# Performance work log

Measured on AMD Instinct MI355X. Metric: run time of the kernel, lower is better.

The kernel has to match this reference:

```python
import jax, jax.numpy as jnp
import numpy as np

B, T, N, DIN, U, K, C = 32, 256, 128, 16, 64, 2, 4
M = K + 1  # num diffusion matrices per support (I, P, 2P^2-I, ...)


def setup_inputs() -> dict:
    key = jax.random.key(0)
    ks = jax.random.split(key, 10)
    w = lambda k, shape: jax.random.normal(k, shape, jnp.float32) * 0.05
    inp = {}
    inp["input_seq"] = jax.random.normal(ks[0], (B, T, N, DIN), jnp.float32)
    inp["seq_lengths"] = jax.random.randint(ks[1], (B,), 1, T + 1)
    # scaled dense support (graph laplacian surrogate) for numerical stability
    inp["support"] = jax.random.normal(ks[2], (N, N), jnp.float32) / N
    inp["W0_gate"] = w(ks[3], ((DIN + U) * M, 2 * U))
    inp["b0_gate"] = jnp.ones((2 * U,), jnp.float32)  # bias_start=1.0
    inp["W0_cand"] = w(ks[4], ((DIN + U) * M, U))
    inp["b0_cand"] = jnp.zeros((U,), jnp.float32)
    inp["W1_gate"] = w(ks[5], (2 * U * M, 2 * U))
    inp["b1_gate"] = jnp.ones((2 * U,), jnp.float32)
    inp["W1_cand"] = w(ks[6], (2 * U * M, U))
    inp["b1_cand"] = jnp.zeros((U,), jnp.float32)
    inp["W_fc"] = w(ks[7], (U, C))
    inp["b_fc"] = jnp.zeros((C,), jnp.float32)
    return inp


def _gconv(x, support, W, b):
    # x: (B, N, Cin). Chebyshev-style diffusion: [x, Px, 2P(Px)-x, ...]
    x0 = x
    x1 = jnp.einsum('mn,bnc->bmc', support, x0)
    xs = [x0, x1]
    for _ in range(2, K + 1):
        x2 = 2.0 * jnp.einsum('mn,bnc->bmc', support, x1) - x0
        xs.append(x2)
        x0, x1 = x1, x2
    # stack on last axis -> (B, N, Cin, M) -> (B, N, Cin*M), matching the
    # torch reshape order (input feature major, matrix minor)
    xc = jnp.stack(xs, axis=-1).reshape(x.shape[0], x.shape[1], -1)
    return xc @ W + b


def _cell(x, h, support, Wg, bg, Wc, bc):
    # x: (B,N,Din), h: (B,N,U)
    val = jax.nn.sigmoid(_gconv(jnp.concatenate([x, h], axis=-1), support, Wg, bg))
    r, u = jnp.split(val, 2, axis=-1)
    c = jnp.tanh(_gconv(jnp.concatenate([x, r * h], axis=-1), support, Wc, bc))
    return u * h + (1.0 - u) * c


def _run_layer(x_seq, support, Wg, bg, Wc, bc):
    # x_seq: (T, B, N, D)
    def step(h, x):
        h2 = _cell(x, h, support, Wg, bg, Wc, bc)
        return h2, h2
    h0 = jnp.zeros((x_seq.shape[1], N, U), x_seq.dtype)
    _, out = jax.lax.scan(step, h0, x_seq)
    return out  # (T, B, N, U)


def reference(input_seq, seq_lengths, support, W0_gate, b0_gate, W0_cand, b0_cand,
              W1_gate, b1_gate, W1_cand, b1_cand, W_fc, b_fc):
    x = jnp.transpose(input_seq, (1, 0, 2, 3))  # (T,B,N,DIN)
    h1 = _run_layer(x, support, W0_gate, b0_gate, W0_cand, b0_cand)
    h2 = _run_layer(h1, support, W1_gate, b1_gate, W1_cand, b1_cand)
    out_seq = jnp.transpose(h2, (1, 0, 2, 3))  # (B,T,N,U)
    idx = seq_lengths - 1  # last relevant timestep per sequence
    last = out_seq[jnp.arange(out_seq.shape[0]), idx]  # (B,N,U)
    # dropout is identity in eval mode
    logits = jax.nn.relu(last) @ W_fc + b_fc  # (B,N,C)
    return jnp.max(logits, axis=1)  # max-pool over nodes -> (B,C)
```

## Files before the change

### kernel.cpp

```cpp
#include <hip/hip_runtime.h>

#define B_   32
#define T_   256
#define N_   128
#define DIN_ 16
#define U_   64

#define PD 456
#define PT 136
#define LDS_BYTES ((N_*PD + N_*PT)*2)

#define WT0G_OFF 0
#define WT0C_OFF (128*256)
#define WT1G_OFF (WT0C_OFF + 64*256)
#define WT1C_OFF (WT1G_OFF + 128*384)
#define WT_TOTAL (WT1C_OFF + 64*384)
#define S2_OFF   WT_TOTAL
#define FIFO_OFF (S2_OFF + 128*128)
#define FIFO_SLOT(bb,tt) (FIFO_OFF + ((bb)*8 + ((tt)&7))*8192)
#define FLG_BYTE ((FIFO_OFF + 32*8*8192)*2)

typedef __attribute__((ext_vector_type(8))) short bfrag;
typedef __attribute__((ext_vector_type(4))) float ffrag;
typedef __attribute__((ext_vector_type(4))) unsigned short us4;
typedef __attribute__((ext_vector_type(2))) unsigned short us2;
typedef unsigned long long ull;

#define SYNC() asm volatile("s_waitcnt lgkmcnt(0)\n\ts_barrier" ::: "memory")
#define MFMA16(a,b,c) __builtin_amdgcn_mfma_f32_16x16x32_bf16(a,b,c,0,0,0)

__device__ __forceinline__ unsigned short f2b(float x) {
  union { float f; unsigned u; } v; v.f = x;
  return (unsigned short)((v.u + 0x7fffu + ((v.u >> 16) & 1u)) >> 16);
}
__device__ __forceinline__ float sigm(float x) {
  float e = __expf(-x);
  return __builtin_amdgcn_rcpf(1.f + e);
}
__device__ __forceinline__ float tanh_(float x) {
  float e = __expf(2.f * x);
  return 1.f - 2.f * __builtin_amdgcn_rcpf(1.f + e);
}

__device__ __forceinline__ float wval0(const float* w, int ncol, int co, int k) {
  if (k < 16)  return w[(k*3+0)*ncol+co] - w[(k*3+2)*ncol+co];
  if (k < 48)  { int j=k-16, c=j>>1;
                 return (j&1) ? 2.f*w[(c*3+2)*ncol+co] : w[(c*3+1)*ncol+co]; }
  if (k < 64)  return 0.f;
  if (k < 128) { int c=16+(k-64); return w[(c*3+0)*ncol+co] - w[(c*3+2)*ncol+co]; }
  { int j=k-128, c=16+(j>>1);
    return (j&1) ? 2.f*w[(c*3+2)*ncol+co] : w[(c*3+1)*ncol+co]; }
}
__device__ __forceinline__ float wval1(const float* w, int ncol, int co, int k) {
  if (k < 64)  return w[(k*3+0)*ncol+co] - w[(k*3+2)*ncol+co];
  if (k < 192) { int j=k-64, c=j>>1;
                 return (j&1) ? 2.f*w[(c*3+2)*ncol+co] : w[(c*3+1)*ncol+co]; }
  if (k < 256) { int c=64+(k-192); return w[(c*3+0)*ncol+co] - w[(c*3+2)*ncol+co]; }
  { int j=k-256, c=64+(j>>1);
    return (j&1) ? 2.f*w[(c*3+2)*ncol+co] : w[(c*3+1)*ncol+co]; }
}
__device__ __forceinline__ float wval0c(const float* w, int ncol, int co, int k) {
  if (k < 64)  return wval0(w, ncol, co, k);
  if (k < 192) return wval0(w, ncol, co, k + 64);
  return wval0(w, ncol, co, k - 128);
}
__device__ __forceinline__ float wval1c(const float* w, int ncol, int co, int k) {
  if (k < 192) return wval1(w, ncol, co, k);
  if (k < 320) return wval1(w, ncol, co, k + 64);
  return wval1(w, ncol, co, k - 128);
}

__global__ void setup_wt(const float* __restrict__ w0g, const float* __restrict__ w0c,
                         const float* __restrict__ w1g, const float* __restrict__ w1c,
                         unsigned short* __restrict__ wt) {
  int i = blockIdx.x * blockDim.x + threadIdx.x;
  if (i >= WT_TOTAL) return;
  float v;
  if (i < WT0C_OFF)      { int co = i >> 8, k = i & 255;                 v = wval0 (w0g, 128, co, k); }
  else if (i < WT1G_OFF) { int j = i - WT0C_OFF; v = wval0c(w0c, 64, j >> 8, j & 255); }
  else if (i < WT1C_OFF) { int j = i - WT1G_OFF; v = wval1 (w1g, 128, j / 384, j % 384); }
  else                   { int j = i - WT1C_OFF; v = wval1c(w1c, 64, j / 384, j % 384); }
  wt[i] = f2b(v);
}

__global__ void setup_s2(const float* __restrict__ sup, unsigned short* __restrict__ s2) {
  int idx = blockIdx.x * blockDim.x + threadIdx.x;
  int i = idx >> 7, j = idx & 127;
  float acc = 0.f;
#pragma unroll 4
  for (int k = 0; k < 128; ++k) acc += sup[i*128 + k] * sup[k*128 + j];
  s2[idx] = f2b(acc);
}

__global__ void zero_flags(unsigned short* __restrict__ wt) {
  int* flg = (int*)((char*)wt + FLG_BYTE);
  if (threadIdx.x < 64) flg[threadIdx.x] = 0;
}

template<int KT>
__device__ __forceinline__ void gateR(ffrag (&acc)[4][2],
    const bfrag (&bwr)[KT], const bfrag (&bwu)[KT],
    const unsigned short* __restrict__ arowB, const int lq) {
#pragma unroll
  for (int ks = 0; ks < KT; ++ks) {
    bfrag a[4];
#pragma unroll
    for (int i = 0; i < 4; ++i)
      a[i] = *(const bfrag*)&arowB[16*i*PD + 32*ks + 8*lq];
#pragma unroll
    for (int i = 0; i < 4; ++i) {
      acc[i][0] = MFMA16(a[i], bwr[ks], acc[i][0]);
      acc[i][1] = MFMA16(a[i], bwu[ks], acc[i][1]);
    }
  }
}
template<int KT>
__device__ __forceinline__ void candR(ffrag (&acc)[4], bfrag (&bw)[4],
    const unsigned short* __restrict__ arowB, const int (&kofs)[KT],
    const unsigned short* __restrict__ bpc, const int lq) {
#pragma unroll
  for (int ks = 0; ks < KT; ++ks) {
    const int k = ks & 3;
    bfrag a[4];
#pragma unroll
    for (int i = 0; i < 4; ++i)
      a[i] = *(const bfrag*)&arowB[16*i*PD + kofs[ks] + 8*lq];
    bfrag bc = bw[k];
    if (ks + 4 < KT) bw[k] = *(const bfrag*)&bpc[32*(ks+4) + 8*lq];
#pragma unroll
    for (int i = 0; i < 4; ++i) acc[i] = MFMA16(a[i], bc, acc[i]);
  }
}

__global__ __launch_bounds__(512, 2) void dcgru(
    const float* __restrict__ xseq, const int* __restrict__ slen,
    const float* __restrict__ sup,
    const float* __restrict__ b0g, const float* __restrict__ b0c,
    const float* __restrict__ b1g, const float* __restrict__ b1c,
    const float* __restrict__ wfc, const float* __restrict__ bfc,
    unsigned short* __restrict__ wt, float* __restrict__ out) {
  extern __shared__ unsigned short lds[];
  unsigned short* diffb = lds;
  unsigned short* difT  = lds + N_*PD;
  const int b    = (blockIdx.x & 7) | ((blockIdx.x >> 4) << 3);
  const int eta  = (blockIdx.x >> 3) & 1;
  const int tid  = threadIdx.x;
  const int w    = tid >> 6;
  const int j    = w & 3;
  const int g    = w >> 2;
  const int ln   = tid & 15;
  const int lq   = (tid >> 4) & 3;
  const int L    = slen[b];
  int* flg  = (int*)((char*)wt + FLG_BYTE);
  int* prod = flg + b;
  int* cons = flg + 32 + b;
  const unsigned short* __restrict__ arowB = diffb + (64*g + ln)*PD;
  const ffrag fz = {0.f, 0.f, 0.f, 0.f};

  bfrag Sf[4], S2f[4];
#pragma unroll
  for (int ks = 0; ks < 4; ++ks) {
    const float* pS = sup + (16*w + ln)*N_ + 32*ks + 8*lq;
    union { bfrag v; unsigned short u[8]; } tmp;
#pragma unroll
    for (int jj = 0; jj < 8; ++jj) tmp.u[jj] = f2b(pS[jj]);
    Sf[ks] = tmp.v;
    S2f[ks] = *(const bfrag*)&wt[S2_OFF + (16*w + ln)*N_ + 32*ks + 8*lq];
  }

  auto diffuse = [&](int nt, int colc) {
    bfrag bf[4];
#pragma unroll
    for (int ks = 0; ks < 4; ++ks)
      bf[ks] = *(const bfrag*)&difT[(16*nt + ln)*PT + 32*ks + 8*lq];
    ffrag a1 = fz, a2 = fz;
#pragma unroll
    for (int ks = 0; ks < 4; ++ks) {
      a1 = MFMA16(Sf[ks],  bf[ks], a1);
      a2 = MFMA16(S2f[ks], bf[ks], a2);
    }
    const int n0 = 16*w + 4*lq;
    const int col = colc + 2*ln;
#pragma unroll
    for (int r = 0; r < 4; ++r) {
      us2 pq = {f2b(a1[r]), f2b(a2[r])};
      *(us2*)&diffb[(n0 + r)*PD + col] = pq;
    }
  };
  auto dumpCell = [&](ffrag (&v)[4], int colBase, int rowBase) {
    const int chh = 16*j + ln;
#pragma unroll
    for (int i = 0; i < 4; ++i) {
      const int n0 = 64*g + 16*i + 4*lq;
      unsigned short sv[4];
#pragma unroll
      for (int r = 0; r < 4; ++r) sv[r] = f2b(v[i][r]);
#pragma unroll
      for (int r = 0; r < 4; ++r) diffb[(n0 + r)*PD + colBase + chh] = sv[r];
      us4 q = {sv[0], sv[1], sv[2], sv[3]};
      *(us4*)&difT[(rowBase + chh)*PT + n0] = q;
    }
  };
  auto prebC = [&](bfrag (&bw)[4], const unsigned short* bpc) {
#pragma unroll
    for (int k = 0; k < 4; ++k) bw[k] = *(const bfrag*)&bpc[32*k + 8*lq];
  };
  auto waitge = [&](int* p, int seq) {
    if ((tid & 63) == 0) {
      int it = 0;
      while (__hip_atomic_load(p, __ATOMIC_RELAXED, __HIP_MEMORY_SCOPE_AGENT) < seq) {
        __builtin_amdgcn_s_sleep(1);
        if (++it > (1 << 24)) break;
      }
    }
  };

  bfrag bw4[4];

  if (eta == 0) {
    bfrag bwr[8], bwu[8];
    {
      const unsigned short* bpr = wt + WT0G_OFF + (16*j      + ln)*256;
      const unsigned short* bpu = wt + WT0G_OFF + (16*(4+j)  + ln)*256;
#pragma unroll
      for (int ks = 0; ks < 8; ++ks) {
        bwr[ks] = *(const bfrag*)&bpr[32*ks + 8*lq];
        bwu[ks] = *(const bfrag*)&bpu[32*ks + 8*lq];
      }
    }
    const unsigned short* bpc = wt + WT0C_OFF + (16*j + ln)*256;
    const float bgr = b0g[16*j + ln], bgu = b0g[64 + 16*j + ln];
    const float bcv = b0c[16*j + ln];
    const int kofs0[8] = {0, 32, 128, 160, 192, 224, 256, 288};
    ffrag h0m[4] = {fz, fz, fz, fz};

    for (int i = tid; i < N_*16; i += 512)
      diffb[(i >> 4)*PD + 48 + (i & 15)] = 0;
    float4 xv = *(const float4*)&xseq[(size_t)(b*T_)*N_*DIN_ + 4*tid];

#pragma clang loop unroll(disable)
    for (int t = 0; t < L; ++t) {
      {
        const int node = tid >> 2, c = 4*(tid & 3);
        unsigned short s0 = f2b(xv.x), s1 = f2b(xv.y), s2 = f2b(xv.z), s3 = f2b(xv.w);
        us4 q = {s0, s1, s2, s3};
        *(us4*)&diffb[node*PD + c] = q;
        difT[(c+0)*PT + node] = s0; difT[(c+1)*PT + node] = s1;
        difT[(c+2)*PT + node] = s2; difT[(c+3)*PT + node] = s3;
        dumpCell(h0m, 64, 16);
        int tn = t + 1 < L ? t + 1 : L - 1;
        xv = *(const float4*)&xseq[(size_t)(b*T_ + tn)*N_*DIN_ + 4*tid];
      }
      SYNC();
      diffuse(0, 16);  diffuse(1, 128); diffuse(2, 160);
      diffuse(3, 192); diffuse(4, 224);
      SYNC();
      ffrag u0s[4], rh[4];
      {
        ffrag ga[4][2] = {{fz, fz}, {fz, fz}, {fz, fz}, {fz, fz}};
        gateR<8>(ga, bwr, bwu, arowB, lq);
#pragma unroll
        for (int i = 0; i < 4; ++i)
#pragma unroll
          for (int r = 0; r < 4; ++r) {
            float rr = sigm(ga[i][0][r] + bgr);
            rh[i][r]  = rr * h0m[i][r];
            u0s[i][r] = sigm(ga[i][1][r] + bgu);
          }
      }
      dumpCell(rh, 256, 16);
      prebC(bw4, bpc);
      SYNC();
      diffuse(1, 128); diffuse(2, 160); diffuse(3, 192); diffuse(4, 224);
      SYNC();
      {
        ffrag ca[4] = {fz, fz, fz, fz};
        candR<8>(ca, bw4, arowB, kofs0, bpc, lq);
#pragma unroll
        for (int i = 0; i < 4; ++i)
#pragma unroll
          for (int r = 0; r < 4; ++r) {
            float cc = tanh_(ca[i][r] + bcv);
            float uu = u0s[i][r];
            h0m[i][r] = uu*h0m[i][r] + (1.f - uu)*cc;
          }
      }
      if (t >= 8) waitge(cons, t - 7);
      {
        unsigned short* slot = wt + FIFO_SLOT(b, t);
        const int chh = 16*j + ln;
#pragma unroll
        for (int i = 0; i < 4; ++i) {
          const int n0 = 64*g + 16*i + 4*lq;
          us4 q = {f2b(h0m[i][0]), f2b(h0m[i][1]), f2b(h0m[i][2]), f2b(h0m[i][3])};
          *(us4*)&slot[chh*128 + n0] = q;
        }
      }
      asm volatile("s_waitcnt vmcnt(0)" ::: "memory");
      if ((tid & 63) == 0)
        __hip_atomic_fetch_add(prod, 1, __ATOMIC_RELEASE, __HIP_MEMORY_SCOPE_AGENT);
      SYNC();
    }
    return;
  }

  {
    bfrag bwr[12], bwu[12];
    {
      const unsigned short* bpr = wt + WT1G_OFF + (16*j     + ln)*384;
      const unsigned short* bpu = wt + WT1G_OFF + (16*(4+j) + ln)*384;
#pragma unroll
      for (int ks = 0; ks < 12; ++ks) {
        bwr[ks] = *(const bfrag*)&bpr[32*ks + 8*lq];
        bwu[ks] = *(const bfrag*)&bpu[32*ks + 8*lq];
      }
    }
    const unsigned short* bpc = wt + WT1C_OFF + (16*j + ln)*384;
    const float bgr = b1g[16*j + ln], bgu = b1g[64 + 16*j + ln];
    const float bcv = b1c[16*j + ln];
    const int kofs1[12] = {0, 32, 64, 96, 128, 160, 256, 288, 320, 352, 384, 416};
    ffrag h1m[4] = {fz, fz, fz, fz};

#pragma clang loop unroll(disable)
    for (int t = 0; t < L; ++t) {
      waitge(prod, 8*(t + 1));
      {
        const unsigned short* slot = wt + FIFO_SLOT(b, t);
#pragma unroll
        for (int rep = 0; rep < 4; ++rep) {
          const int idx = tid + 512*rep;
          const int ch = idx >> 5, n0 = (idx & 31)*4;
          ull v = __hip_atomic_load((const ull*)&slot[ch*128 + n0],
                                    __ATOMIC_RELAXED, __HIP_MEMORY_SCOPE_AGENT);
          *(ull*)&difT[ch*PT + n0] = v;
          union { ull u; unsigned short s[4]; } cv; cv.u = v;
#pragma unroll
          for (int jj = 0; jj < 4; ++jj) diffb[(n0 + jj)*PD + ch] = cv.s[jj];
        }
        dumpCell(h1m, 192, 64);
      }
      SYNC();
      if (tid == 0)
        __hip_atomic_fetch_add(cons, 1, __ATOMIC_RELEASE, __HIP_MEMORY_SCOPE_AGENT);
      diffuse(0, 64);  diffuse(1, 96);  diffuse(2, 128); diffuse(3, 160);
      diffuse(4, 256); diffuse(5, 288); diffuse(6, 320); diffuse(7, 352);
      SYNC();
      ffrag u1s[4], rh[4];
      {
        ffrag ga[4][2] = {{fz, fz}, {fz, fz}, {fz, fz}, {fz, fz}};
        gateR<12>(ga, bwr, bwu, arowB, lq);
#pragma unroll
        for (int i = 0; i < 4; ++i)
#pragma unroll
          for (int r = 0; r < 4; ++r) {
            float rr = sigm(ga[i][0][r] + bgr);
            rh[i][r]  = rr * h1m[i][r];
            u1s[i][r] = sigm(ga[i][1][r] + bgu);
          }
      }
      dumpCell(rh, 384, 64);
      prebC(bw4, bpc);
      SYNC();
      diffuse(4, 256); diffuse(5, 288); diffuse(6, 320); diffuse(7, 352);
      SYNC();
      {
        ffrag ca[4] = {fz, fz, fz, fz};
        candR<12>(ca, bw4, arowB, kofs1, bpc, lq);
#pragma unroll
        for (int i = 0; i < 4; ++i)
#pragma unroll
          for (int r = 0; r < 4; ++r) {
            float cc = tanh_(ca[i][r] + bcv);
            float uu = u1s[i][r];
            h1m[i][r] = uu*h1m[i][r] + (1.f - uu)*cc;
          }
      }
      SYNC();
    }

    {
      float* hb = (float*)lds;
#pragma unroll
      for (int i = 0; i < 4; ++i)
#pragma unroll
        for (int r = 0; r < 4; ++r) {
          float v = h1m[i][r];
          hb[(64*g + 16*i + 4*lq + r)*U_ + 16*j + ln] = v > 0.f ? v : 0.f;
        }
    }
    __syncthreads();
    float* hb = (float*)lds;
    float* lb = hb + N_*U_;
    if (tid < N_) {
      float lg[4];
#pragma unroll
      for (int jj = 0; jj < 4; ++jj) lg[jj] = bfc[jj];
      for (int ch = 0; ch < U_; ++ch) {
        float v = hb[tid*U_ + ch];
#pragma unroll
        for (int jj = 0; jj < 4; ++jj) lg[jj] += v * wfc[ch*4 + jj];
      }
#pragma unroll
      for (int jj = 0; jj < 4; ++jj) lb[tid*4 + jj] = lg[jj];
    }
    __syncthreads();
    if (tid < 4) {
      float m = lb[tid];
      for (int n = 1; n < N_; ++n) m = fmaxf(m, lb[n*4 + tid]);
      out[b*4 + tid] = m;
    }
  }
}

extern "C" void kernel_launch(void* const* d_in, const int* in_sizes, int n_in,
                              void* d_out, int out_size, void* d_ws, size_t ws_size,
                              hipStream_t stream) {
  const float* xseq = (const float*)d_in[0];
  const int*   slen = (const int*)  d_in[1];
  const float* sup  = (const float*)d_in[2];
  const float* w0g  = (const float*)d_in[3];
  const float* b0g  = (const float*)d_in[4];
  const float* w0c  = (const float*)d_in[5];
  const float* b0c  = (const float*)d_in[6];
  const float* w1g  = (const float*)d_in[7];
  const float* b1g  = (const float*)d_in[8];
  const float* w1c  = (const float*)d_in[9];
  const float* b1c  = (const float*)d_in[10];
  const float* wfc  = (const float*)d_in[11];
  const float* bfc  = (const float*)d_in[12];
  float* out = (float*)d_out;
  unsigned short* wt = (unsigned short*)d_ws;

  (void)hipFuncSetAttribute((const void*)dcgru,
                            hipFuncAttributeMaxDynamicSharedMemorySize, LDS_BYTES);
  zero_flags<<<dim3(1), dim3(64), 0, stream>>>(wt);
  setup_wt<<<dim3((WT_TOTAL + 255)/256), dim3(256), 0, stream>>>(w0g, w0c, w1g, w1c, wt);
  setup_s2<<<dim3(64), dim3(256), 0, stream>>>(sup, wt + S2_OFF);
  dcgru<<<dim3(64), dim3(512), LDS_BYTES, stream>>>(
      xseq, slen, sup, b0g, b0c, b1g, b1c, wfc, bfc, wt, out);
}
```

Baseline: 2.626 ms.

## Move layer-1 input diffusion of h into layer-0 producer and ship via second FIFO

The layer-0 producer workgroup now diffuses its freshly computed hidden state (P·h, 2P²h−h terms) right after each step. It writes those diffused features to a new global FIFO so the layer-1 consumer can load them instead of recomputing four diffusion passes. This rebalances work between the two pipelined stages, which suits a consumer-bound pipeline. The cost is extra global traffic, a shallower FIFO depth (4 instead of 8), extra syncs in the producer, and a changed zero-initialisation of the producer's diffusion buffer.

```diff
diff --git a/kernel.cpp b/kernel.cpp
--- a/kernel.cpp
+++ b/kernel.cpp
@@ -19,6 +19,8 @@
 #define FIFO_OFF (S2_OFF + 128*128)
 #define FIFO_SLOT(bb,tt) (FIFO_OFF + ((bb)*8 + ((tt)&7))*8192)
 #define FLG_BYTE ((FIFO_OFF + 32*8*8192)*2)
+#define FIFO2_OFF (FIFO_OFF + 32*8*8192 + 128)
+#define FIFO2_SLOT(bb,tt) (FIFO2_OFF + ((bb)*4 + ((tt)&3))*16384)
 
 typedef __attribute__((ext_vector_type(8))) short bfrag;
 typedef __attribute__((ext_vector_type(4))) float ffrag;
@@ -234,8 +236,10 @@
     const int kofs0[8] = {0, 32, 128, 160, 192, 224, 256, 288};
     ffrag h0m[4] = {fz, fz, fz, fz};
 
-    for (int i = tid; i < N_*16; i += 512)
-      diffb[(i >> 4)*PD + 48 + (i & 15)] = 0;
+    for (int i = tid; i < N_*208; i += 512) {
+      int row = i / 208, c = i - row*208;
+      diffb[row*PD + 48 + c] = 0;
+    }
     float4 xv = *(const float4*)&xseq[(size_t)(b*T_)*N_*DIN_ + 4*tid];
 
 #pragma clang loop unroll(disable)
@@ -247,13 +251,11 @@
         *(us4*)&diffb[node*PD + c] = q;
         difT[(c+0)*PT + node] = s0; difT[(c+1)*PT + node] = s1;
         difT[(c+2)*PT + node] = s2; difT[(c+3)*PT + node] = s3;
-        dumpCell(h0m, 64, 16);
         int tn = t + 1 < L ? t + 1 : L - 1;
         xv = *(const float4*)&xseq[(size_t)(b*T_ + tn)*N_*DIN_ + 4*tid];
       }
       SYNC();
-      diffuse(0, 16);  diffuse(1, 128); diffuse(2, 160);
-      diffuse(3, 192); diffuse(4, 224);
+      diffuse(0, 16);
       SYNC();
       ffrag u0s[4], rh[4];
       {
@@ -285,7 +287,8 @@
             h0m[i][r] = uu*h0m[i][r] + (1.f - uu)*cc;
           }
       }
-      if (t >= 8) waitge(cons, t - 7);
+      dumpCell(h0m, 64, 16);
+      if (t >= 4) waitge(cons, t - 3);
       {
         unsigned short* slot = wt + FIFO_SLOT(b, t);
         const int chh = 16*j + ln;
@@ -296,10 +299,22 @@
           *(us4*)&slot[chh*128 + n0] = q;
         }
       }
+      SYNC();
+      diffuse(1, 128); diffuse(2, 160); diffuse(3, 192); diffuse(4, 224);
+      SYNC();
+      {
+        unsigned short* slot2 = wt + FIFO2_SLOT(b, t);
+#pragma unroll
+        for (int rep = 0; rep < 8; ++rep) {
+          const int i = tid + 512*rep;
+          const int node = i >> 5, off = (i & 31)*4;
+          ull v = *(const ull*)&diffb[node*PD + 128 + off];
+          *(ull*)&slot2[node*128 + off] = v;
+        }
+      }
       asm volatile("s_waitcnt vmcnt(0)" ::: "memory");
       if ((tid & 63) == 0)
         __hip_atomic_fetch_add(prod, 1, __ATOMIC_RELEASE, __HIP_MEMORY_SCOPE_AGENT);
-      SYNC();
     }
     return;
   }
@@ -332,17 +347,24 @@
           const int ch = idx >> 5, n0 = (idx & 31)*4;
           ull v = __hip_atomic_load((const ull*)&slot[ch*128 + n0],
                                     __ATOMIC_RELAXED, __HIP_MEMORY_SCOPE_AGENT);
-          *(ull*)&difT[ch*PT + n0] = v;
           union { ull u; unsigned short s[4]; } cv; cv.u = v;
 #pragma unroll
           for (int jj = 0; jj < 4; ++jj) diffb[(n0 + jj)*PD + ch] = cv.s[jj];
         }
+        const unsigned short* slot2 = wt + FIFO2_SLOT(b, t);
+#pragma unroll
+        for (int rep = 0; rep < 8; ++rep) {
+          const int i = tid + 512*rep;
+          const int node = i >> 5, off = (i & 31)*4;
+          ull v = __hip_atomic_load((const ull*)&slot2[node*128 + off],
+                                    __ATOMIC_RELAXED, __HIP_MEMORY_SCOPE_AGENT);
+          *(ull*)&diffb[node*PD + 64 + off] = v;
+        }
         dumpCell(h1m, 192, 64);
       }
       SYNC();
       if (tid == 0)
         __hip_atomic_fetch_add(cons, 1, __ATOMIC_RELEASE, __HIP_MEMORY_SCOPE_AGENT);
-      diffuse(0, 64);  diffuse(1, 96);  diffuse(2, 128); diffuse(3, 160);
       diffuse(4, 256); diffuse(5, 288); diffuse(6, 320); diffuse(7, 352);
       SYNC();
       ffrag u1s[4], rh[4];
```

Result: faster. 2.521 ms (-4.0%).

## Ship pre-diffused layer-0 outputs through FIFO and software-pipeline both layers

Applied to the files above, without the earlier changes.

Layer 0 now computes the diffusion of its new hidden state plus the next timestep's input diffusion at the end of each step, and sends the already-diffused rows (h, Ph, P²h terms) to layer 1 through a larger 4-deep FIFO. Layer 1 no longer recomputes the diffusion of the incoming layer-0 output, and fetches the next slot while finishing the current step. Diffusion of x(t+1) is overlapped with h's diffusion, which cuts a barrier round per step. The cost is three times more global FIFO traffic per step, a shallower ring, and per-wave consumer counting.

```diff
diff --git a/kernel.cpp b/kernel.cpp
--- a/kernel.cpp
+++ b/kernel.cpp
@@ -16,9 +16,9 @@
 #define WT1C_OFF (WT1G_OFF + 128*384)
 #define WT_TOTAL (WT1C_OFF + 64*384)
 #define S2_OFF   WT_TOTAL
-#define FIFO_OFF (S2_OFF + 128*128)
-#define FIFO_SLOT(bb,tt) (FIFO_OFF + ((bb)*8 + ((tt)&7))*8192)
-#define FLG_BYTE ((FIFO_OFF + 32*8*8192)*2)
+#define FIFO2_OFF (S2_OFF + 128*128)
+#define FIFO2_SLOT(bb,tt) (FIFO2_OFF + ((bb)*4 + ((tt)&3))*24576)
+#define FLG_BYTE ((FIFO2_OFF + 32*4*24576)*2)
 
 typedef __attribute__((ext_vector_type(8))) short bfrag;
 typedef __attribute__((ext_vector_type(4))) float ffrag;
@@ -156,6 +156,8 @@
   int* cons = flg + 32 + b;
   const unsigned short* __restrict__ arowB = diffb + (64*g + ln)*PD;
   const ffrag fz = {0.f, 0.f, 0.f, 0.f};
+  const int fnode = tid & 127;
+  const int fkb   = tid >> 7;
 
   bfrag Sf[4], S2f[4];
 #pragma unroll
@@ -234,27 +236,29 @@
     const int kofs0[8] = {0, 32, 128, 160, 192, 224, 256, 288};
     ffrag h0m[4] = {fz, fz, fz, fz};
 
-    for (int i = tid; i < N_*16; i += 512)
-      diffb[(i >> 4)*PD + 48 + (i & 15)] = 0;
+    auto stageX = [&](float4 v) {
+      const int node = tid >> 2, c = 4*(tid & 3);
+      unsigned short s0 = f2b(v.x), s1 = f2b(v.y), s2 = f2b(v.z), s3 = f2b(v.w);
+      us4 q = {s0, s1, s2, s3};
+      *(us4*)&diffb[node*PD + c] = q;
+      difT[(c+0)*PT + node] = s0; difT[(c+1)*PT + node] = s1;
+      difT[(c+2)*PT + node] = s2; difT[(c+3)*PT + node] = s3;
+    };
+
+    for (int i = tid; i < N_*208; i += 512) {
+      int row = i / 208, c = i - row*208;
+      diffb[row*PD + 48 + c] = 0;
+    }
     float4 xv = *(const float4*)&xseq[(size_t)(b*T_)*N_*DIN_ + 4*tid];
+    stageX(xv);
+    { int tn = 1 < L ? 1 : L - 1;
+      xv = *(const float4*)&xseq[(size_t)(b*T_ + tn)*N_*DIN_ + 4*tid]; }
+    SYNC();
+    diffuse(0, 16);
+    SYNC();
 
 #pragma clang loop unroll(disable)
     for (int t = 0; t < L; ++t) {
-      {
-        const int node = tid >> 2, c = 4*(tid & 3);
-        unsigned short s0 = f2b(xv.x), s1 = f2b(xv.y), s2 = f2b(xv.z), s3 = f2b(xv.w);
-        us4 q = {s0, s1, s2, s3};
-        *(us4*)&diffb[node*PD + c] = q;
-        difT[(c+0)*PT + node] = s0; difT[(c+1)*PT + node] = s1;
-        difT[(c+2)*PT + node] = s2; difT[(c+3)*PT + node] = s3;
-        dumpCell(h0m, 64, 16);
-        int tn = t + 1 < L ? t + 1 : L - 1;
-        xv = *(const float4*)&xseq[(size_t)(b*T_ + tn)*N_*DIN_ + 4*tid];
-      }
-      SYNC();
-      diffuse(0, 16);  diffuse(1, 128); diffuse(2, 160);
-      diffuse(3, 192); diffuse(4, 224);
-      SYNC();
       ffrag u0s[4], rh[4];
       {
         ffrag ga[4][2] = {{fz, fz}, {fz, fz}, {fz, fz}, {fz, fz}};
@@ -285,15 +289,22 @@
             h0m[i][r] = uu*h0m[i][r] + (1.f - uu)*cc;
           }
       }
-      if (t >= 8) waitge(cons, t - 7);
+      dumpCell(h0m, 64, 16);
+      if (t >= 4) waitge(cons, 8*(t - 3));
+      SYNC();
+      diffuse(1, 128); diffuse(2, 160); diffuse(3, 192); diffuse(4, 224);
+      stageX(xv);
+      { int tn = t + 2 < L ? t + 2 : L - 1;
+        xv = *(const float4*)&xseq[(size_t)(b*T_ + tn)*N_*DIN_ + 4*tid]; }
+      SYNC();
+      diffuse(0, 16);
       {
-        unsigned short* slot = wt + FIFO_SLOT(b, t);
-        const int chh = 16*j + ln;
-#pragma unroll
-        for (int i = 0; i < 4; ++i) {
-          const int n0 = 64*g + 16*i + 4*lq;
-          us4 q = {f2b(h0m[i][0]), f2b(h0m[i][1]), f2b(h0m[i][2]), f2b(h0m[i][3])};
-          *(us4*)&slot[chh*128 + n0] = q;
+        unsigned short* slot2 = wt + FIFO2_SLOT(b, t);
+#pragma unroll
+        for (int r = 0; r < 12; ++r) {
+          const int k = fkb + 4*r;
+          ull v = *(const ull*)&diffb[fnode*PD + 64 + 4*k];
+          *(ull*)&slot2[k*128*4 + fnode*4] = v;
         }
       }
       asm volatile("s_waitcnt vmcnt(0)" ::: "memory");
@@ -321,30 +332,30 @@
     const int kofs1[12] = {0, 32, 64, 96, 128, 160, 256, 288, 320, 352, 384, 416};
     ffrag h1m[4] = {fz, fz, fz, fz};
 
+    auto recvSlot = [&](int t) {
+      const unsigned short* slot2 = wt + FIFO2_SLOT(b, t);
+#pragma unroll
+      for (int r = 0; r < 12; ++r) {
+        const int k = fkb + 4*r;
+        ull v = __hip_atomic_load((const ull*)&slot2[k*128*4 + fnode*4],
+                                  __ATOMIC_RELAXED, __HIP_MEMORY_SCOPE_AGENT);
+        *(ull*)&diffb[fnode*PD + 4*k] = v;
+      }
+      asm volatile("s_waitcnt vmcnt(0)" ::: "memory");
+      if ((tid & 63) == 0)
+        __hip_atomic_fetch_add(cons, 1, __ATOMIC_RELEASE, __HIP_MEMORY_SCOPE_AGENT);
+    };
+
+    for (int i = tid; i < N_*192; i += 512) {
+      int row = i / 192, c = i - row*192;
+      diffb[row*PD + 192 + c] = 0;
+    }
+    waitge(prod, 8);
+    recvSlot(0);
+    SYNC();
+
 #pragma clang loop unroll(disable)
     for (int t = 0; t < L; ++t) {
-      waitge(prod, 8*(t + 1));
-      {
-        const unsigned short* slot = wt + FIFO_SLOT(b, t);
-#pragma unroll
-        for (int rep = 0; rep < 4; ++rep) {
-          const int idx = tid + 512*rep;
-          const int ch = idx >> 5, n0 = (idx & 31)*4;
-          ull v = __hip_atomic_load((const ull*)&slot[ch*128 + n0],
-                                    __ATOMIC_RELAXED, __HIP_MEMORY_SCOPE_AGENT);
-          *(ull*)&difT[ch*PT + n0] = v;
-          union { ull u; unsigned short s[4]; } cv; cv.u = v;
-#pragma unroll
-          for (int jj = 0; jj < 4; ++jj) diffb[(n0 + jj)*PD + ch] = cv.s[jj];
-        }
-        dumpCell(h1m, 192, 64);
-      }
-      SYNC();
-      if (tid == 0)
-        __hip_atomic_fetch_add(cons, 1, __ATOMIC_RELEASE, __HIP_MEMORY_SCOPE_AGENT);
-      diffuse(0, 64);  diffuse(1, 96);  diffuse(2, 128); diffuse(3, 160);
-      diffuse(4, 256); diffuse(5, 288); diffuse(6, 320); diffuse(7, 352);
-      SYNC();
       ffrag u1s[4], rh[4];
       {
         ffrag ga[4][2] = {{fz, fz}, {fz, fz}, {fz, fz}, {fz, fz}};
@@ -374,6 +385,13 @@
             float uu = u1s[i][r];
             h1m[i][r] = uu*h1m[i][r] + (1.f - uu)*cc;
           }
+      }
+      dumpCell(h1m, 192, 64);
+      SYNC();
+      diffuse(4, 256); diffuse(5, 288); diffuse(6, 320); diffuse(7, 352);
+      if (t + 1 < L) {
+        waitge(prod, 8*(t + 2));
+        recvSlot(t + 1);
       }
       SYNC();
     }
```

Measured after the change: 3.044 ms. 15.9% more time.
